# Performance work log

Measured on AMD Instinct MI355X. Metric: run time of the kernel, lower is better.

Reference implementation:

```python
import jax, jax.numpy as jnp
import numpy as np
from jax import lax

B, T, D_IN = 64, 4096, 64
D_EMB, H = 24, 128


def setup_inputs() -> dict:
    key = jax.random.key(0)
    ks = jax.random.split(key, 8)
    s = 0.01  # matches RandomNormal(stddev=0.01) style init
    return {
        "x": jax.random.normal(ks[0], (B, T, D_IN), jnp.float32),
        "W_emb": jax.random.normal(ks[1], (D_IN, D_EMB), jnp.float32) * s,
        "b_emb": jnp.zeros((D_EMB,), jnp.float32),
        "W_f": jax.random.normal(ks[2], (D_EMB + H, H), jnp.float32) * s,
        "b_f": jnp.ones((H,), jnp.float32),  # forget bias init to ones (as in source)
        "W_i": jax.random.normal(ks[3], (D_EMB + H, H), jnp.float32) * s,
        "b_i": jnp.zeros((H,), jnp.float32),
        "W_c": jax.random.normal(ks[4], (D_EMB + H, H), jnp.float32) * s,
        "b_c": jnp.zeros((H,), jnp.float32),
        "W_o": jax.random.normal(ks[5], (D_EMB + H, H), jnp.float32) * s,
        "b_o": jnp.zeros((H,), jnp.float32),
        "W_out": jax.random.normal(ks[6], (H, 1), jnp.float32) * s,
        "b_out": jnp.zeros((1,), jnp.float32),
    }


def reference(x, W_emb, b_emb, W_f, b_f, W_i, b_i, W_c, b_c, W_o, b_o, W_out, b_out):
    # embedding: Dense(24, sigmoid) applied per timestep
    e = jax.nn.sigmoid(jnp.einsum('btd,de->bte', x, W_emb) + b_emb)  # [B,T,24]
    e_t = jnp.swapaxes(e, 0, 1)  # [T,B,24] for scan over time

    def step(carry, et):
        h, c = carry
        z = jnp.concatenate([et, h], axis=-1)            # [B, 24+128]
        f = jax.nn.sigmoid(z @ W_f + b_f)
        i = jax.nn.sigmoid(z @ W_i + b_i)
        g = jnp.tanh(z @ W_c + b_c)
        o = jax.nn.sigmoid(z @ W_o + b_o)
        c_new = c * f + i * g
        h_new = jnp.tanh(c_new) * o
        return (h_new, c_new), None

    h0 = jnp.zeros((x.shape[0], W_f.shape[1]), x.dtype)
    c0 = jnp.zeros_like(h0)
    (hT, _), _ = lax.scan(step, (h0, c0), e_t)
    return jax.nn.sigmoid(hT @ W_out + b_out)  # [B,1]
```

## Files before the change

kernel.cpp:

```cpp
#include <hip/hip_runtime.h>
#include <stdint.h>

namespace {
constexpr int kB = 64, kT = 4096, kDin = 64, kDe = 24, kH = 128;
constexpr int kCh = 16;
constexpr int kNCh = kT / kCh;
constexpr int kRowU = 16;
constexpr int kPS = 20;

typedef __attribute__((ext_vector_type(8))) _Float16 frag8;
typedef __attribute__((ext_vector_type(4))) float v4f;
typedef __attribute__((ext_vector_type(8))) int v8i;
union H2U { uint32_t u; _Float16 s[2]; };

__device__ __forceinline__ float rcp_fast(float x){
#if __has_builtin(__builtin_amdgcn_rcpf)
  return __builtin_amdgcn_rcpf(x);
#else
  return 1.0f / x;
#endif
}
__device__ __forceinline__ float sigmoid_f(float x){
  return rcp_fast(1.0f + __expf(-x));
}
__device__ __forceinline__ float tanh_f(float x){
  return 1.0f - 2.0f * rcp_fast(1.0f + __expf(2.0f * x));
}
__device__ __forceinline__ uint32_t pack2(float lo, float hi){
  H2U u; u.s[0] = (_Float16)lo; u.s[1] = (_Float16)hi; return u.u;
}
__device__ __forceinline__ uint32_t sw_fp8(float x){
  union{float f; uint32_t u;} v; v.f = x;
  uint32_t s = (v.u >> 24) & 0x80u;
  float a = fabsf(x);
  if (a < 0.0009765625f) return s;
  if (a > 448.0f) a = 448.0f;
  int e; float m = frexpf(a, &e);
  int E = e - 1 + 7;
  uint32_t bits;
  if (E <= 0){
    int q = (int)(a * 512.0f + 0.5f); if (q > 7) q = 7; bits = (uint32_t)q;
  } else {
    int q = (int)(m * 16.0f + 0.5f);
    if (q == 16){ q = 8; ++E; }
    if (E > 15) { E = 15; q = 14; }
    bits = ((uint32_t)E << 3) | ((uint32_t)q & 7u);
  }
  return s | bits;
}
template <bool HI>
__device__ __forceinline__ uint32_t fp8pair(float a, float b, uint32_t old){
#if __has_builtin(__builtin_amdgcn_cvt_pk_fp8_f32)
  return (uint32_t)__builtin_amdgcn_cvt_pk_fp8_f32(a, b, (int)old, HI);
#else
  uint32_t p = sw_fp8(a) | (sw_fp8(b) << 8);
  return HI ? ((old & 0x0000ffffu) | (p << 16)) : ((old & 0xffff0000u) | p);
#endif
}
}

__global__ __launch_bounds__(256) void emb_kernel(
    const float* __restrict__ x, const float* __restrict__ W,
    const float* __restrict__ bias, uint32_t* __restrict__ e_out)
{
  int r = blockIdx.x * blockDim.x + threadIdx.x;
  if (r >= kB * kT) return;
  const float4* xr = (const float4*)(x + (size_t)r * kDin);
  float acc[kDe];
#pragma unroll
  for (int k = 0; k < kDe; ++k) acc[k] = bias[k];
#pragma unroll 4
  for (int d4 = 0; d4 < kDin / 4; ++d4){
    float4 xv = xr[d4];
    const float* w0 = W + (size_t)(d4 * 4) * kDe;
#pragma unroll
    for (int k = 0; k < kDe; ++k) acc[k] += xv.x * w0[k];
#pragma unroll
    for (int k = 0; k < kDe; ++k) acc[k] += xv.y * w0[kDe + k];
#pragma unroll
    for (int k = 0; k < kDe; ++k) acc[k] += xv.z * w0[2 * kDe + k];
#pragma unroll
    for (int k = 0; k < kDe; ++k) acc[k] += xv.w * w0[3 * kDe + k];
  }
  uint32_t p[12];
#pragma unroll
  for (int k = 0; k < 12; ++k)
    p[k] = pack2(sigmoid_f(acc[2 * k]), sigmoid_f(acc[2 * k + 1]));
  uint4* dst = (uint4*)(e_out + (size_t)r * kRowU);
  dst[0] = make_uint4(p[0], p[1], p[2],  p[3]);
  dst[1] = make_uint4(p[4], p[5], p[6],  p[7]);
  dst[2] = make_uint4(p[8], p[9], p[10], p[11]);
  dst[3] = make_uint4(0u, 0u, 0u, 0u);
}

__global__ __launch_bounds__(512, 1) void lstm_kernel(
    const uint32_t* __restrict__ e_ws,
    const float* __restrict__ W_f, const float* __restrict__ b_f,
    const float* __restrict__ W_i, const float* __restrict__ b_i,
    const float* __restrict__ W_c, const float* __restrict__ b_c,
    const float* __restrict__ W_o, const float* __restrict__ b_o,
    const float* __restrict__ W_out, const float* __restrict__ b_out,
    float* __restrict__ out)
{
  __shared__ __align__(16) float preh[4 * kH * kPS];
  __shared__ __align__(16) uint32_t elds[kCh * kRowU];
  __shared__ __align__(64) uint32_t hfp8[2 * 32];
  __shared__ float red[8];

  const int b  = blockIdx.x;
  const int t0 = threadIdx.x;
  const int w  = t0 >> 6;
  const int l  = t0 & 63;
  const int q  = l >> 4;
  const int cl = l & 15;
  const int u  = w * 16 + cl;

  const float* Wg[4] = {W_f, W_i, W_c, W_o};

  v8i B8[4];
#pragma unroll
  for (int g = 0; g < 4; ++g){
#pragma unroll
    for (int r = 0; r < 8; ++r){
      const float* col = Wg[g] + (size_t)(24 + q * 32 + r * 4) * kH + u;
      uint32_t reg = fp8pair<false>(col[0] * 64.0f, col[kH] * 64.0f, 0u);
      reg = fp8pair<true>(col[2 * kH] * 64.0f, col[3 * kH] * 64.0f, reg);
      B8[g][r] = (int)reg;
    }
  }

  frag8 Bp[4];
  float biasC[4] = {b_f[u], b_i[u], b_c[u], b_o[u]};
#pragma unroll
  for (int g = 0; g < 4; ++g){
#pragma unroll
    for (int j = 0; j < 8; ++j){
      int k = q * 8 + j;
      Bp[g][j] = (_Float16)((k < kDe) ? Wg[g][(size_t)k * kH + u] : 0.0f);
    }
  }

  const uint4* e4 = (const uint4*)e_ws;
  const size_t bbase = (size_t)b * kT * 4;

  auto do_pregemm = [&](){
    frag8 Ae = *(const frag8*)&elds[cl * kRowU + q * 4];
#pragma unroll
    for (int g = 0; g < 4; ++g){
      v4f c; c[0] = biasC[g]; c[1] = biasC[g]; c[2] = biasC[g]; c[3] = biasC[g];
      v4f d = __builtin_amdgcn_mfma_f32_16x16x32_f16(Ae, Bp[g], c, 0, 0, 0);
      *(v4f*)&preh[(g * kH + u) * kPS + q * 4] = d;
    }
  };
  float pb[4][kCh];
  auto load_pb = [&](){
#pragma unroll
    for (int g = 0; g < 4; ++g){
      const v4f* src = (const v4f*)&preh[(g * kH + u) * kPS];
#pragma unroll
      for (int r = 0; r < 4; ++r){
        v4f t = src[r];
        pb[g][4*r+0] = t[0]; pb[g][4*r+1] = t[1];
        pb[g][4*r+2] = t[2]; pb[g][4*r+3] = t[3];
      }
    }
  };

  uint4 pre4;
  if (t0 < 64) ((uint4*)elds)[t0] = e4[bbase + t0];
  if (t0 < 32) hfp8[t0] = 0u;
  __syncthreads();
  do_pregemm();
  load_pb();
  if (t0 < 64 && kNCh > 1) pre4 = e4[bbase + (size_t)kCh * 4 + t0];

  float cst = 0.0f, h_last = 0.0f;
  const v4f zero4 = {0.0f, 0.0f, 0.0f, 0.0f};

#pragma unroll 1
  for (int cc = 0; cc < kNCh; ++cc){
#pragma unroll
    for (int s = 0; s < kCh; ++s){
      const int cur = (cc * kCh + s) & 1, nxt = cur ^ 1;

      v8i A = *(const v8i*)&hfp8[cur * 32 + q * 8];

      v4f a0 = __builtin_amdgcn_mfma_scale_f32_16x16x128_f8f6f4(
                   A, B8[0], zero4, 0, 0, 0, 121, 0, 121);
      v4f a1 = __builtin_amdgcn_mfma_scale_f32_16x16x128_f8f6f4(
                   A, B8[1], zero4, 0, 0, 0, 121, 0, 121);
      v4f a2 = __builtin_amdgcn_mfma_scale_f32_16x16x128_f8f6f4(
                   A, B8[2], zero4, 0, 0, 0, 121, 0, 121);
      v4f a3 = __builtin_amdgcn_mfma_scale_f32_16x16x128_f8f6f4(
                   A, B8[3], zero4, 0, 0, 0, 121, 0, 121);

      float f  = sigmoid_f(a0[0] + pb[0][s]);
      float ig = sigmoid_f(a1[0] + pb[1][s]);
      float gg = tanh_f(a2[0] + pb[2][s]);
      float og = sigmoid_f(a3[0] + pb[3][s]);
      cst    = fmaf(cst, f, ig * gg);
      h_last = tanh_f(cst) * og;
      if (l < 16){
        uint32_t byte = fp8pair<false>(h_last * 64.0f, h_last * 64.0f, 0u) & 0xffu;
        ((uint8_t*)&hfp8[nxt * 32])[u] = (uint8_t)byte;
      }
      if (s == kCh - 1 && cc + 1 < kNCh && t0 < 64) ((uint4*)elds)[t0] = pre4;
      __syncthreads();
    }

    if (cc + 1 < kNCh){
      do_pregemm();
      load_pb();
      if (t0 < 64 && cc + 2 < kNCh)
        pre4 = e4[bbase + (size_t)(cc + 2) * kCh * 4 + t0];
    }
  }

  float partial = (l < 16) ? h_last * W_out[u] : 0.0f;
#pragma unroll
  for (int off = 1; off <= 32; off <<= 1) partial += __shfl_xor(partial, off, 64);
  if (l == 0) red[w] = partial;
  __syncthreads();
  if (t0 == 0){
    float acc = b_out[0];
#pragma unroll
    for (int k = 0; k < 8; ++k) acc += red[k];
    out[b] = sigmoid_f(acc);
  }
}

extern "C" void kernel_launch(void* const* d_in, const int* in_sizes, int n_in,
                              void* d_out, int out_size, void* d_ws, size_t ws_size,
                              hipStream_t stream){
  const float* x     = (const float*)d_in[0];
  const float* W_emb = (const float*)d_in[1];
  const float* b_emb = (const float*)d_in[2];
  const float* W_f   = (const float*)d_in[3];
  const float* b_f   = (const float*)d_in[4];
  const float* W_i   = (const float*)d_in[5];
  const float* b_i   = (const float*)d_in[6];
  const float* W_c   = (const float*)d_in[7];
  const float* b_c   = (const float*)d_in[8];
  const float* W_o   = (const float*)d_in[9];
  const float* b_o   = (const float*)d_in[10];
  const float* W_out = (const float*)d_in[11];
  const float* b_out = (const float*)d_in[12];
  float* out = (float*)d_out;
  uint32_t* e_ws = (uint32_t*)d_ws;

  const int rows = kB * kT;
  emb_kernel<<<(rows + 255) / 256, 256, 0, stream>>>(x, W_emb, b_emb, e_ws);
  lstm_kernel<<<kB, 512, 0, stream>>>(e_ws, W_f, b_f, W_i, b_i, W_c, b_c,
                                      W_o, b_o, W_out, b_out, out);
}
```

Before: 1.541 ms.

## Process two batch rows per LSTM block and store pre-activations as fp16

Each 512-thread block now runs the recurrence for two batch elements at once. Lanes 0-31 and 32-63 of every wave each take one sequence, and each step issues eight independent scaled-FP8 MFMAs on separate double-buffered h tiles, with the MFMAs moved after the barrier. The input pre-GEMM results are packed to fp16 in LDS to fit the doubled buffers, which lowers precision of the pre-activations. The launch uses half as many blocks; this is meant to make better use of idle lanes and MFMA slots but leaves the serial step chain per block unchanged.

```diff
diff --git a/kernel.cpp b/kernel.cpp
--- a/kernel.cpp
+++ b/kernel.cpp
@@ -6,7 +6,6 @@
 constexpr int kCh = 16;
 constexpr int kNCh = kT / kCh;
 constexpr int kRowU = 16;
-constexpr int kPS = 20;
 
 typedef __attribute__((ext_vector_type(8))) _Float16 frag8;
 typedef __attribute__((ext_vector_type(4))) float v4f;
@@ -102,18 +101,19 @@
     const float* __restrict__ W_out, const float* __restrict__ b_out,
     float* __restrict__ out)
 {
-  __shared__ __align__(16) float preh[4 * kH * kPS];
-  __shared__ __align__(16) uint32_t elds[kCh * kRowU];
-  __shared__ __align__(64) uint32_t hfp8[2 * 32];
-  __shared__ float red[8];
-
-  const int b  = blockIdx.x;
+  __shared__ __align__(16) uint32_t preh16[2 * 4 * kH * 8];
+  __shared__ __align__(16) uint32_t elds[2 * kCh * kRowU];
+  __shared__ __align__(64) uint32_t hfp8[4 * 32];
+  __shared__ float red[16];
+
+  const int b0 = blockIdx.x * 2;
   const int t0 = threadIdx.x;
   const int w  = t0 >> 6;
   const int l  = t0 & 63;
   const int q  = l >> 4;
   const int cl = l & 15;
   const int u  = w * 16 + cl;
+  const int ch = l >> 5;
 
   const float* Wg[4] = {W_f, W_i, W_c, W_o};
 
@@ -141,91 +141,116 @@
   }
 
   const uint4* e4 = (const uint4*)e_ws;
-  const size_t bbase = (size_t)b * kT * 4;
-
-  auto do_pregemm = [&](){
-    frag8 Ae = *(const frag8*)&elds[cl * kRowU + q * 4];
+  const int erow  = t0 & 63;
+  const size_t ebase = (size_t)(b0 + (t0 >> 6)) * (kT * 4) + erow;
+
+  auto do_pregemm = [&](int c){
+    frag8 Ae = *(const frag8*)&elds[c * (kCh * kRowU) + cl * kRowU + q * 4];
 #pragma unroll
     for (int g = 0; g < 4; ++g){
-      v4f c; c[0] = biasC[g]; c[1] = biasC[g]; c[2] = biasC[g]; c[3] = biasC[g];
-      v4f d = __builtin_amdgcn_mfma_f32_16x16x32_f16(Ae, Bp[g], c, 0, 0, 0);
-      *(v4f*)&preh[(g * kH + u) * kPS + q * 4] = d;
+      v4f cc4; cc4[0] = biasC[g]; cc4[1] = biasC[g]; cc4[2] = biasC[g]; cc4[3] = biasC[g];
+      v4f d = __builtin_amdgcn_mfma_f32_16x16x32_f16(Ae, Bp[g], cc4, 0, 0, 0);
+      uint2 pk; pk.x = pack2(d[0], d[1]); pk.y = pack2(d[2], d[3]);
+      *(uint2*)&preh16[((c * 4 + g) * kH + u) * 8 + q * 2] = pk;
     }
   };
+
   float pb[4][kCh];
+  auto unpk = [](uint32_t v, float& a, float& b){
+    H2U t; t.u = v; a = (float)t.s[0]; b = (float)t.s[1];
+  };
   auto load_pb = [&](){
 #pragma unroll
     for (int g = 0; g < 4; ++g){
-      const v4f* src = (const v4f*)&preh[(g * kH + u) * kPS];
-#pragma unroll
-      for (int r = 0; r < 4; ++r){
-        v4f t = src[r];
-        pb[g][4*r+0] = t[0]; pb[g][4*r+1] = t[1];
-        pb[g][4*r+2] = t[2]; pb[g][4*r+3] = t[3];
-      }
+      const uint4* src = (const uint4*)&preh16[((ch * 4 + g) * kH + u) * 8];
+      uint4 lo = src[0], hi = src[1];
+      unpk(lo.x, pb[g][0],  pb[g][1]);  unpk(lo.y, pb[g][2],  pb[g][3]);
+      unpk(lo.z, pb[g][4],  pb[g][5]);  unpk(lo.w, pb[g][6],  pb[g][7]);
+      unpk(hi.x, pb[g][8],  pb[g][9]);  unpk(hi.y, pb[g][10], pb[g][11]);
+      unpk(hi.z, pb[g][12], pb[g][13]); unpk(hi.w, pb[g][14], pb[g][15]);
     }
   };
 
-  uint4 pre4;
-  if (t0 < 64) ((uint4*)elds)[t0] = e4[bbase + t0];
-  if (t0 < 32) hfp8[t0] = 0u;
+  uint4 pre4 = make_uint4(0u, 0u, 0u, 0u);
+  if (t0 < 128) ((uint4*)elds)[t0] = e4[ebase];
   __syncthreads();
-  do_pregemm();
+  do_pregemm(0); do_pregemm(1);
   load_pb();
-  if (t0 < 64 && kNCh > 1) pre4 = e4[bbase + (size_t)kCh * 4 + t0];
+  if (t0 < 128 && kNCh > 1) pre4 = e4[ebase + (size_t)kCh * 4];
 
   float cst = 0.0f, h_last = 0.0f;
   const v4f zero4 = {0.0f, 0.0f, 0.0f, 0.0f};
+  v4f aA0 = zero4, aA1 = zero4, aA2 = zero4, aA3 = zero4;
+  v4f aB0 = zero4, aB1 = zero4, aB2 = zero4, aB3 = zero4;
 
 #pragma unroll 1
   for (int cc = 0; cc < kNCh; ++cc){
 #pragma unroll
     for (int s = 0; s < kCh; ++s){
-      const int cur = (cc * kCh + s) & 1, nxt = cur ^ 1;
-
-      v8i A = *(const v8i*)&hfp8[cur * 32 + q * 8];
-
-      v4f a0 = __builtin_amdgcn_mfma_scale_f32_16x16x128_f8f6f4(
-                   A, B8[0], zero4, 0, 0, 0, 121, 0, 121);
-      v4f a1 = __builtin_amdgcn_mfma_scale_f32_16x16x128_f8f6f4(
-                   A, B8[1], zero4, 0, 0, 0, 121, 0, 121);
-      v4f a2 = __builtin_amdgcn_mfma_scale_f32_16x16x128_f8f6f4(
-                   A, B8[2], zero4, 0, 0, 0, 121, 0, 121);
-      v4f a3 = __builtin_amdgcn_mfma_scale_f32_16x16x128_f8f6f4(
-                   A, B8[3], zero4, 0, 0, 0, 121, 0, 121);
-
-      float f  = sigmoid_f(a0[0] + pb[0][s]);
-      float ig = sigmoid_f(a1[0] + pb[1][s]);
-      float gg = tanh_f(a2[0] + pb[2][s]);
-      float og = sigmoid_f(a3[0] + pb[3][s]);
+      const int par = s & 1;
+
+      float x0 = (ch ? aB0[0] : aA0[0]) + pb[0][s];
+      float x1 = (ch ? aB1[0] : aA1[0]) + pb[1][s];
+      float x2 = (ch ? aB2[0] : aA2[0]) + pb[2][s];
+      float x3 = (ch ? aB3[0] : aA3[0]) + pb[3][s];
+      float f  = sigmoid_f(x0);
+      float ig = sigmoid_f(x1);
+      float gg = tanh_f(x2);
+      float og = sigmoid_f(x3);
       cst    = fmaf(cst, f, ig * gg);
       h_last = tanh_f(cst) * og;
-      if (l < 16){
+      if (!(l & 16)){
         uint32_t byte = fp8pair<false>(h_last * 64.0f, h_last * 64.0f, 0u) & 0xffu;
-        ((uint8_t*)&hfp8[nxt * 32])[u] = (uint8_t)byte;
+        ((uint8_t*)hfp8)[(ch * 2 + par) * 128 + u] = (uint8_t)byte;
       }
-      if (s == kCh - 1 && cc + 1 < kNCh && t0 < 64) ((uint4*)elds)[t0] = pre4;
+      if (s == kCh - 1 && cc + 1 < kNCh && t0 < 128) ((uint4*)elds)[t0] = pre4;
       __syncthreads();
+
+      v8i Aa = *(const v8i*)&hfp8[(0 + par) * 32 + q * 8];
+      v8i Ab = *(const v8i*)&hfp8[(2 + par) * 32 + q * 8];
+      aA0 = __builtin_amdgcn_mfma_scale_f32_16x16x128_f8f6f4(
+                Aa, B8[0], zero4, 0, 0, 0, 121, 0, 121);
+      aA1 = __builtin_amdgcn_mfma_scale_f32_16x16x128_f8f6f4(
+                Aa, B8[1], zero4, 0, 0, 0, 121, 0, 121);
+      aA2 = __builtin_amdgcn_mfma_scale_f32_16x16x128_f8f6f4(
+                Aa, B8[2], zero4, 0, 0, 0, 121, 0, 121);
+      aA3 = __builtin_amdgcn_mfma_scale_f32_16x16x128_f8f6f4(
+                Aa, B8[3], zero4, 0, 0, 0, 121, 0, 121);
+      aB0 = __builtin_amdgcn_mfma_scale_f32_16x16x128_f8f6f4(
+                Ab, B8[0], zero4, 0, 0, 0, 121, 0, 121);
+      aB1 = __builtin_amdgcn_mfma_scale_f32_16x16x128_f8f6f4(
+                Ab, B8[1], zero4, 0, 0, 0, 121, 0, 121);
+      aB2 = __builtin_amdgcn_mfma_scale_f32_16x16x128_f8f6f4(
+                Ab, B8[2], zero4, 0, 0, 0, 121, 0, 121);
+      aB3 = __builtin_amdgcn_mfma_scale_f32_16x16x128_f8f6f4(
+                Ab, B8[3], zero4, 0, 0, 0, 121, 0, 121);
     }
 
     if (cc + 1 < kNCh){
-      do_pregemm();
+      do_pregemm(0); do_pregemm(1);
       load_pb();
-      if (t0 < 64 && cc + 2 < kNCh)
-        pre4 = e4[bbase + (size_t)(cc + 2) * kCh * 4 + t0];
-    }
-  }
-
-  float partial = (l < 16) ? h_last * W_out[u] : 0.0f;
-#pragma unroll
-  for (int off = 1; off <= 32; off <<= 1) partial += __shfl_xor(partial, off, 64);
-  if (l == 0) red[w] = partial;
+      if (t0 < 128 && cc + 2 < kNCh)
+        pre4 = e4[ebase + (size_t)(cc + 2) * kCh * 4];
+    }
+  }
+
+  float partial = (!(l & 16)) ? h_last * W_out[u] : 0.0f;
+#pragma unroll
+  for (int off = 1; off <= 16; off <<= 1) partial += __shfl_xor(partial, off, 64);
+  if (l == 0)  red[w]     = partial;
+  if (l == 32) red[8 + w] = partial;
   __syncthreads();
   if (t0 == 0){
     float acc = b_out[0];
 #pragma unroll
     for (int k = 0; k < 8; ++k) acc += red[k];
-    out[b] = sigmoid_f(acc);
+    out[b0] = sigmoid_f(acc);
+  }
+  if (t0 == 1){
+    float acc = b_out[0];
+#pragma unroll
+    for (int k = 0; k < 8; ++k) acc += red[8 + k];
+    out[b0 + 1] = sigmoid_f(acc);
   }
 }
 
@@ -250,6 +275,6 @@
 
   const int rows = kB * kT;
   emb_kernel<<<(rows + 255) / 256, 256, 0, stream>>>(x, W_emb, b_emb, e_ws);
-  lstm_kernel<<<kB, 512, 0, stream>>>(e_ws, W_f, b_f, W_i, b_i, W_c, b_c,
-                                      W_o, b_o, W_out, b_out, out);
-}
+  lstm_kernel<<<kB / 2, 512, 0, stream>>>(e_ws, W_f, b_f, W_i, b_i, W_c, b_c,
+                                          W_o, b_o, W_out, b_out, out);
+}
```

After: 2.098 ms. +36.2%, slower.

## Spread gate activations across lane quads and fold exp scaling into weights

Applied to the files above, without the earlier changes.

Each 16-lane quad now evaluates only one gate's nonlinearity, chosen by lane group. The four gate values are then exchanged with ds_bpermute, so each lane does one exp and one reciprocal instead of four. The -log2e (and -2log2e for tanh) factors are folded into the FP8/FP16 weights and biases, which allows raw exp2, and the preactivation buffer per lane shrinks to one gate. The __syncthreads is replaced by an explicit lgkmcnt wait plus s_barrier. Scaling the FP8 weights by larger factors may change quantization error, and the permutes add LDS traffic on the serial critical path.

```diff
diff --git a/kernel.cpp b/kernel.cpp
--- a/kernel.cpp
+++ b/kernel.cpp
@@ -7,6 +7,7 @@
 constexpr int kNCh = kT / kCh;
 constexpr int kRowU = 16;
 constexpr int kPS = 20;
+constexpr float kLog2e = 1.4426950408889634f;
 
 typedef __attribute__((ext_vector_type(8))) _Float16 frag8;
 typedef __attribute__((ext_vector_type(4))) float v4f;
@@ -20,11 +21,15 @@
   return 1.0f / x;
 #endif
 }
+__device__ __forceinline__ float exp2_f(float x){
+#if __has_builtin(__builtin_amdgcn_exp2f)
+  return __builtin_amdgcn_exp2f(x);
+#else
+  return exp2f(x);
+#endif
+}
 __device__ __forceinline__ float sigmoid_f(float x){
   return rcp_fast(1.0f + __expf(-x));
-}
-__device__ __forceinline__ float tanh_f(float x){
-  return 1.0f - 2.0f * rcp_fast(1.0f + __expf(2.0f * x));
 }
 __device__ __forceinline__ uint32_t pack2(float lo, float hi){
   H2U u; u.s[0] = (_Float16)lo; u.s[1] = (_Float16)hi; return u.u;
@@ -57,6 +62,13 @@
   return HI ? ((old & 0x0000ffffu) | (p << 16)) : ((old & 0xffff0000u) | p);
 #endif
 }
+__device__ __forceinline__ void lgkm_barrier(){
+  asm volatile("s_waitcnt lgkmcnt(0)" ::: "memory");
+  __builtin_amdgcn_sched_barrier(0);
+  __builtin_amdgcn_s_barrier();
+  __builtin_amdgcn_sched_barrier(0);
+  asm volatile("" ::: "memory");
+}
 }
 
 __global__ __launch_bounds__(256) void emb_kernel(
@@ -116,29 +128,37 @@
   const int u  = w * 16 + cl;
 
   const float* Wg[4] = {W_f, W_i, W_c, W_o};
+  const float* bgp[4] = {b_f, b_i, b_c, b_o};
+  const float scl[4] = {-kLog2e, -kLog2e, -2.0f * kLog2e, -kLog2e};
 
   v8i B8[4];
 #pragma unroll
   for (int g = 0; g < 4; ++g){
+    const float sc = scl[g] * 64.0f;
 #pragma unroll
     for (int r = 0; r < 8; ++r){
       const float* col = Wg[g] + (size_t)(24 + q * 32 + r * 4) * kH + u;
-      uint32_t reg = fp8pair<false>(col[0] * 64.0f, col[kH] * 64.0f, 0u);
-      reg = fp8pair<true>(col[2 * kH] * 64.0f, col[3 * kH] * 64.0f, reg);
+      uint32_t reg = fp8pair<false>(col[0] * sc, col[kH] * sc, 0u);
+      reg = fp8pair<true>(col[2 * kH] * sc, col[3 * kH] * sc, reg);
       B8[g][r] = (int)reg;
     }
   }
 
   frag8 Bp[4];
-  float biasC[4] = {b_f[u], b_i[u], b_c[u], b_o[u]};
+  float biasC[4];
 #pragma unroll
   for (int g = 0; g < 4; ++g){
+    biasC[g] = bgp[g][u] * scl[g];
 #pragma unroll
     for (int j = 0; j < 8; ++j){
       int k = q * 8 + j;
-      Bp[g][j] = (_Float16)((k < kDe) ? Wg[g][(size_t)k * kH + u] : 0.0f);
-    }
-  }
+      Bp[g][j] = (_Float16)((k < kDe) ? Wg[g][(size_t)k * kH + u] * scl[g] : 0.0f);
+    }
+  }
+
+  const float Sg = (q == 2) ? 2.0f : 1.0f;
+  const float Tg = (q == 2) ? -1.0f : 0.0f;
+  const int aF = cl * 4, aI = (16 + cl) * 4, aG = (32 + cl) * 4, aO = (48 + cl) * 4;
 
   const uint4* e4 = (const uint4*)e_ws;
   const size_t bbase = (size_t)b * kT * 4;
@@ -152,17 +172,13 @@
       *(v4f*)&preh[(g * kH + u) * kPS + q * 4] = d;
     }
   };
-  float pb[4][kCh];
+  float pb[kCh];
   auto load_pb = [&](){
-#pragma unroll
-    for (int g = 0; g < 4; ++g){
-      const v4f* src = (const v4f*)&preh[(g * kH + u) * kPS];
-#pragma unroll
-      for (int r = 0; r < 4; ++r){
-        v4f t = src[r];
-        pb[g][4*r+0] = t[0]; pb[g][4*r+1] = t[1];
-        pb[g][4*r+2] = t[2]; pb[g][4*r+3] = t[3];
-      }
+    const v4f* src = (const v4f*)&preh[(q * kH + u) * kPS];
+#pragma unroll
+    for (int r = 0; r < 4; ++r){
+      v4f t = src[r];
+      pb[4*r+0] = t[0]; pb[4*r+1] = t[1]; pb[4*r+2] = t[2]; pb[4*r+3] = t[3];
     }
   };
 
@@ -194,18 +210,29 @@
       v4f a3 = __builtin_amdgcn_mfma_scale_f32_16x16x128_f8f6f4(
                    A, B8[3], zero4, 0, 0, 0, 121, 0, 121);
 
-      float f  = sigmoid_f(a0[0] + pb[0][s]);
-      float ig = sigmoid_f(a1[0] + pb[1][s]);
-      float gg = tanh_f(a2[0] + pb[2][s]);
-      float og = sigmoid_f(a3[0] + pb[3][s]);
-      cst    = fmaf(cst, f, ig * gg);
-      h_last = tanh_f(cst) * og;
+      float t01 = (q == 0) ? a0[0] : a1[0];
+      float t23 = (q == 2) ? a2[0] : a3[0];
+      float aq  = (q < 2) ? t01 : t23;
+      float xg  = aq + pb[s];
+      float rr  = rcp_fast(1.0f + exp2_f(xg));
+      float gv  = fmaf(rr, Sg, Tg);
+
+      int vi = __float_as_int(gv);
+      float fA = __int_as_float(__builtin_amdgcn_ds_bpermute(aF, vi));
+      float iA = __int_as_float(__builtin_amdgcn_ds_bpermute(aI, vi));
+      float gA = __int_as_float(__builtin_amdgcn_ds_bpermute(aG, vi));
+      float oA = __int_as_float(__builtin_amdgcn_ds_bpermute(aO, vi));
+
+      cst = fmaf(cst, fA, iA * gA);
+      float rh = rcp_fast(1.0f + exp2_f(-2.0f * kLog2e * cst));
+      h_last = fmaf(rh, 2.0f, -1.0f) * oA;
+
       if (l < 16){
         uint32_t byte = fp8pair<false>(h_last * 64.0f, h_last * 64.0f, 0u) & 0xffu;
         ((uint8_t*)&hfp8[nxt * 32])[u] = (uint8_t)byte;
       }
       if (s == kCh - 1 && cc + 1 < kNCh && t0 < 64) ((uint4*)elds)[t0] = pre4;
-      __syncthreads();
+      lgkm_barrier();
     }
 
     if (cc + 1 < kNCh){
```

Result: faster. 1.464 ms (-5.0%).
